# Kernel tuning notes

Hardware: AMD Instinct MI355X
Metric: run time of the kernel (lower is better)

Reference implementation:

```python
import jax, jax.numpy as jnp
import numpy as np

DIM = 1024
HEADS = 16
HEAD_DIM = DIM // HEADS
SCALE = HEAD_DIM ** -0.5


def setup_inputs() -> dict:
    key = jax.random.key(0)
    ks = jax.random.split(key, 6)
    B, N, C = 2, 2048, DIM
    s = C ** -0.5
    return {
        "x": jax.random.normal(ks[0], (B, N, C), dtype=jnp.float32),
        "Wq": jax.random.normal(ks[1], (C, C), dtype=jnp.float32) * s,
        "Wk": jax.random.normal(ks[2], (C, C), dtype=jnp.float32) * s,
        "Wv": jax.random.normal(ks[3], (C, C), dtype=jnp.float32) * s,
        "Wo": jax.random.normal(ks[4], (C, C), dtype=jnp.float32) * s,
        "bo": jax.random.normal(ks[5], (C,), dtype=jnp.float32) * 0.02,
    }


def reference(x, Wq, Wk, Wv, Wo, bo):
    B, N, C = x.shape
    H, D = HEADS, HEAD_DIM
    # q/k/v linears (no bias), reshape to [B, H, N, D]
    q = (x @ Wq.T).reshape(B, N, H, D).transpose(0, 2, 1, 3)
    k = (x @ Wk.T).reshape(B, N, H, D).transpose(0, 2, 1, 3)
    v = (x @ Wv.T).reshape(B, N, H, D).transpose(0, 2, 1, 3)
    attn = jnp.einsum("bhnd,bhmd->bhnm", q, k) * SCALE  # [B,H,N,N]
    attn = jax.nn.softmax(attn, axis=-1)
    out = jnp.einsum("bhnm,bhmd->bhnd", attn, v)  # [B,H,N,D]
    out = out.transpose(0, 2, 1, 3).reshape(B, N, C)
    out = out @ Wo.T + bo  # proj (dropout p=0 in eval -> identity)
    return out
```

## Files before the change

### kernel.cpp

```cpp
#include <hip/hip_runtime.h>
#include <stdint.h>

typedef __attribute__((ext_vector_type(8))) _Float16 half8;
typedef __attribute__((ext_vector_type(8))) unsigned short ushort8;
typedef __attribute__((ext_vector_type(4))) float f32x4;
typedef unsigned short u16;

#define AS1C(p) ((const __attribute__((address_space(1))) void*)(p))
#define AS3(p)  ((__attribute__((address_space(3))) void*)(p))

#define PIPE_WAIT(n) do { asm volatile("s_waitcnt vmcnt(" #n ")" ::: "memory"); \
  __builtin_amdgcn_s_barrier(); __builtin_amdgcn_sched_barrier(0); } while (0)

__device__ __forceinline__ f32x4 mfma_k32(half8 a, half8 b, f32x4 c) {
  return __builtin_amdgcn_mfma_f32_16x16x32_f16(a, b, c, 0, 0, 0);
}
__device__ __forceinline__ u16 f2h(float f) {
  return __builtin_bit_cast(u16, (_Float16)f);
}
__device__ __forceinline__ float fexp2(float x) {
  return __builtin_amdgcn_exp2f(x);
}
__device__ __forceinline__ unsigned int pk2h(float a, float b) {
  return __builtin_bit_cast(unsigned int, __builtin_amdgcn_cvt_pkrtz(a, b));
}
__device__ __forceinline__ int fsz(int r) {
  return (((r & 3) | (((r >> 3) & 1) << 2)) << 4);
}

__global__ __launch_bounds__(256) void k_convert(
    const float* __restrict__ x, const float* __restrict__ wq,
    const float* __restrict__ wk, const float* __restrict__ wv,
    const float* __restrict__ wo,
    u16* __restrict__ xb, u16* __restrict__ wqkvb, u16* __restrict__ wob) {
  size_t t = (size_t)blockIdx.x * 256 + threadIdx.x;
  size_t e = t * 8;
  const float* src;
  u16* dst;
  if (e < 4194304u)      { src = x  + e;            dst = xb    + e; }
  else if (e < 5242880u) { src = wq + (e-4194304u); dst = wqkvb + (e-4194304u); }
  else if (e < 6291456u) { src = wk + (e-5242880u); dst = wqkvb + (e-4194304u); }
  else if (e < 7340032u) { src = wv + (e-6291456u); dst = wqkvb + (e-4194304u); }
  else                   { src = wo + (e-7340032u); dst = wob   + (e-7340032u); }
  float4 a = *(const float4*)src;
  float4 b = *(const float4*)(src + 4);
  ushort8 o;
  o[0]=f2h(a.x); o[1]=f2h(a.y); o[2]=f2h(a.z); o[3]=f2h(a.w);
  o[4]=f2h(b.x); o[5]=f2h(b.y); o[6]=f2h(b.z); o[7]=f2h(b.w);
  *(ushort8*)dst = o;
}

__global__ __launch_bounds__(512) void k_gemm_qkv(
    const u16* __restrict__ xb, const u16* __restrict__ wqkvb,
    u16* __restrict__ qk, u16* __restrict__ vt) {
  __shared__ u16 lA[3 * 4096];
  __shared__ u16 lB[3 * 4096];
  char* lAc = (char*)lA;
  char* lBc = (char*)lB;
  const int lid = blockIdx.x;
  const int xcd = lid & 7, idx = lid >> 3;
  const int pr = idx / 12, pc = idx % 12;
  const int row0 = (((xcd & 3) << 3) + pr) << 7;
  const int col0 = ((xcd >> 2) * 12 + pc) << 7;

  const int tid = threadIdx.x;
  const int w = tid >> 6, lane = tid & 63;
  const int wm = (w & 1) * 64, wn = (w >> 1) * 32;
  const int l15 = lane & 15, l4 = lane >> 4;
  f32x4 acc[4][2];
#pragma unroll
  for (int i = 0; i < 4; ++i)
#pragma unroll
    for (int j = 0; j < 2; ++j) acc[i][j] = (f32x4){0.f, 0.f, 0.f, 0.f};

  const int lrow = lane >> 2;
  const int lcb  = (lane & 3) << 4;
  const char* Abase = (const char*)xb + (size_t)row0 * 2048;
  const char* Bbase = (const char*)wqkvb + (size_t)col0 * 2048;

  auto stage = [&](int buf, int kt) {
    int r = (w << 4) + lrow;
    __builtin_amdgcn_global_load_lds(AS1C(Abase + (size_t)r * 2048 + kt * 64 + lcb),
                                     AS3(lAc + buf * 8192 + w * 1024), 16, 0, 0);
    __builtin_amdgcn_global_load_lds(AS1C(Bbase + (size_t)r * 2048 + kt * 64 + lcb),
                                     AS3(lBc + buf * 8192 + w * 1024), 16, 0, 0);
  };
  auto compute = [&](int buf) {
    const char* A = lAc + buf * 8192;
    const char* B = lBc + buf * 8192;
    half8 af[4], bf[2];
#pragma unroll
    for (int mi = 0; mi < 4; ++mi)
      af[mi] = *(const half8*)(A + (wm + mi * 16 + l15) * 64 + (l4 << 4));
#pragma unroll
    for (int ni = 0; ni < 2; ++ni)
      bf[ni] = *(const half8*)(B + (wn + ni * 16 + l15) * 64 + (l4 << 4));
#pragma unroll
    for (int mi = 0; mi < 4; ++mi)
#pragma unroll
      for (int ni = 0; ni < 2; ++ni)
        acc[mi][ni] = mfma_k32(af[mi], bf[ni], acc[mi][ni]);
  };

  stage(0, 0);
  stage(1, 1);
  for (int k3 = 0; k3 < 30; k3 += 3) {
    PIPE_WAIT(2); stage(2, k3 + 2); compute(0);
    PIPE_WAIT(2); stage(0, k3 + 3); compute(1);
    PIPE_WAIT(2); stage(1, k3 + 4); compute(2);
  }
  PIPE_WAIT(2); compute(0);
  PIPE_WAIT(0); compute(1);

  const int rbase = row0 + wm + (l4 << 2);
  const int cbase = col0 + wn + l15;
  const bool isQ = (col0 < 1024);
  const bool isV = (col0 >= 2048);
#pragma unroll
  for (int mi = 0; mi < 4; ++mi) {
#pragma unroll
    for (int ni = 0; ni < 2; ++ni) {
      const int col = cbase + ni * 16;
      if (!isV) {
#pragma unroll
        for (int r = 0; r < 4; ++r) {
          int row = rbase + mi * 16 + r;
          float v = acc[mi][ni][r];
          if (isQ) v *= 0.18033688f;
          qk[(size_t)row * 2048 + col] = f2h(v);
        }
      } else {
        const int jj = col - 2048;
        const int h = jj >> 6, d = jj & 63;
        const int row = rbase + mi * 16;
        const int b = row >> 11, n = row & 2047;
        u16 pk[4];
#pragma unroll
        for (int r = 0; r < 4; ++r) pk[r] = f2h(acc[mi][ni][r]);
        *(uint2*)&vt[(size_t)(((b << 4) + h) * 64 + d) * 2048 + n] = *(uint2*)pk;
      }
    }
  }
}

__global__ __launch_bounds__(512) void k_attn(
    const u16* __restrict__ qk, const u16* __restrict__ vt, u16* __restrict__ ao) {
  __shared__ u16 KV[6][4096];
  char* L = (char*)&KV[0][0];
  const int lid = blockIdx.x;
  const int xcd = lid & 7, sub = lid >> 3;
  const int bh = (xcd << 2) + (sub >> 4);
  const int qt = sub & 15;
  const int b = bh >> 4, h = bh & 15;
  const int w = threadIdx.x >> 6, lane = threadIdx.x & 63;
  const int l15 = lane & 15, l4 = lane >> 4;

  const int qrow = (b << 11) + (qt << 7) + (w << 4) + l15;
  half8 qf[2];
  qf[0] = *(const half8*)(qk + (size_t)qrow * 2048 + h * 64 + (l4 << 3));
  qf[1] = *(const half8*)(qk + (size_t)qrow * 2048 + h * 64 + 32 + (l4 << 3));

  half8 vones8;
#pragma unroll
  for (int j = 0; j < 8; ++j) vones8[j] = (_Float16)1.0f;

  const int lrow = lane >> 3;
  const int lcb  = (lane & 7) << 4;
  const char* Kbase = (const char*)qk + (size_t)(b << 11) * 4096 + 2048 + h * 128;
  const char* Vbase = (const char*)vt + (size_t)(bh * 64) * 4096;

  const int rr0 = (w << 3) + lrow;
  const int sc0 = lcb ^ fsz(rr0);
  const char* kg0 = Kbase + (size_t)rr0 * 4096 + sc0;
  const char* vg0 = Vbase + (size_t)rr0 * 4096 + sc0;
  const int kd0 = w * 1024;

  const int keybase = ((l15 >> 2) << 3) + (l15 & 3);
  const int kswz = fsz(keybase);
  const int vswz = (((l15 & 3) | (((l15 >> 3) & 1) << 2)) << 4);
  int koff[8], voff[8];
#pragma unroll
  for (int nt = 0; nt < 4; ++nt) {
    const int key = keybase + ((nt & 1) << 2) + ((nt >> 1) << 5);
    koff[2 * nt]     = key * 128 + ((l4 << 4) ^ kswz);
    koff[2 * nt + 1] = key * 128 + (((l4 << 4) + 64) ^ kswz);
  }
#pragma unroll
  for (int dt = 0; dt < 4; ++dt) {
    const int d = dt * 16 + l15;
    voff[2 * dt]     = 24576 + d * 128 + ((l4 << 4) ^ vswz);
    voff[2 * dt + 1] = 24576 + d * 128 + (((l4 << 4) + 64) ^ vswz);
  }

  f32x4 acc_o[4];
  f32x4 acc_l = (f32x4){0.f, 0.f, 0.f, 0.f};
#pragma unroll
  for (int dt = 0; dt < 4; ++dt) acc_o[dt] = (f32x4){0.f, 0.f, 0.f, 0.f};

  auto stage = [&](int buf) {
    __builtin_amdgcn_global_load_lds(AS1C(kg0), AS3(L + buf * 8192 + kd0), 16, 0, 0);
    __builtin_amdgcn_global_load_lds(AS1C(vg0), AS3(L + 24576 + buf * 8192 + kd0), 16, 0, 0);
    kg0 += 262144; vg0 += 128;
  };

  auto compute = [&](int bu) {
    const char* Lb = L + bu * 8192;

    f32x4 s[4];
    __builtin_amdgcn_s_setprio(1);
#pragma unroll
    for (int nt = 0; nt < 4; ++nt) {
      half8 k0 = *(const half8*)(Lb + koff[2 * nt]);
      half8 k1 = *(const half8*)(Lb + koff[2 * nt + 1]);
      f32x4 z = (f32x4){0.f, 0.f, 0.f, 0.f};
      z = mfma_k32(k0, qf[0], z);
      s[nt] = mfma_k32(k1, qf[1], z);
    }
    __builtin_amdgcn_s_setprio(0);

    half8 pb[2];
#pragma unroll
    for (int p = 0; p < 2; ++p) {
      uint4 pk;
      pk.x = pk2h(fexp2(s[2*p][0]),   fexp2(s[2*p][1]));
      pk.y = pk2h(fexp2(s[2*p][2]),   fexp2(s[2*p][3]));
      pk.z = pk2h(fexp2(s[2*p+1][0]), fexp2(s[2*p+1][1]));
      pk.w = pk2h(fexp2(s[2*p+1][2]), fexp2(s[2*p+1][3]));
      pb[p] = __builtin_bit_cast(half8, pk);
    }

    __builtin_amdgcn_s_setprio(1);
#pragma unroll
    for (int dt = 0; dt < 4; ++dt) {
      half8 v0 = *(const half8*)(Lb + voff[2 * dt]);
      half8 v1 = *(const half8*)(Lb + voff[2 * dt + 1]);
      acc_o[dt] = mfma_k32(v0, pb[0], acc_o[dt]);
      acc_o[dt] = mfma_k32(v1, pb[1], acc_o[dt]);
    }
    acc_l = mfma_k32(vones8, pb[0], acc_l);
    acc_l = mfma_k32(vones8, pb[1], acc_l);
    __builtin_amdgcn_s_setprio(0);
  };

  stage(0);
  stage(1);
  for (int k3 = 0; k3 < 30; k3 += 3) {
    PIPE_WAIT(2); stage(2); compute(0);
    PIPE_WAIT(2); stage(0); compute(1);
    PIPE_WAIT(2); stage(1); compute(2);
  }
  PIPE_WAIT(2); compute(0);
  PIPE_WAIT(0); compute(1);

  const float inv = __builtin_amdgcn_rcpf(acc_l[0]);
  const size_t rowbase = ((size_t)(b << 11) + (qt << 7) + (w << 4) + l15) * 1024 + h * 64;
#pragma unroll
  for (int dt = 0; dt < 4; ++dt) {
    uint2 o;
    o.x = pk2h(acc_o[dt][0] * inv, acc_o[dt][1] * inv);
    o.y = pk2h(acc_o[dt][2] * inv, acc_o[dt][3] * inv);
    *(uint2*)&ao[rowbase + dt * 16 + (l4 << 2)] = o;
  }
}

__global__ __launch_bounds__(256) void k_gemm_proj(
    const u16* __restrict__ aob, const u16* __restrict__ wob,
    const float* __restrict__ bo, float* __restrict__ out) {
  __shared__ u16 lA[3 * 4096];
  __shared__ u16 lB[3 * 2048];
  const int lid = blockIdx.x;
  const int xcd = lid & 7, idx = lid >> 3;
  const int row0 = ((xcd << 2) + (idx >> 4)) << 7;
  const int col0 = (idx & 15) << 6;

  const int tid = threadIdx.x;
  const int w = tid >> 6, lane = tid & 63;
  const int wm = (w >> 1) * 64, wn = (w & 1) * 32;
  const int l15 = lane & 15, l4 = lane >> 4;
  f32x4 acc[4][2];
#pragma unroll
  for (int i = 0; i < 4; ++i)
#pragma unroll
    for (int j = 0; j < 2; ++j) acc[i][j] = (f32x4){0.f, 0.f, 0.f, 0.f};

  const int lrow = lane >> 2;
  const int lcb  = (lane & 3) << 4;
  const char* Abase = (const char*)aob + (size_t)row0 * 2048;
  const char* Bbase = (const char*)wob + (size_t)col0 * 2048;
  char* lAc = (char*)lA;
  char* lBc = (char*)lB;

  auto stage = [&](int buf, int kt) {
#pragma unroll
    for (int i = 0; i < 2; ++i) {
      int c = w + 4 * i;
      int r = c * 16 + lrow;
      __builtin_amdgcn_global_load_lds(AS1C(Abase + (size_t)r * 2048 + kt * 64 + lcb),
                                       AS3(lAc + buf * 8192 + c * 1024), 16, 0, 0);
    }
    int rb = w * 16 + lrow;
    __builtin_amdgcn_global_load_lds(AS1C(Bbase + (size_t)rb * 2048 + kt * 64 + lcb),
                                     AS3(lBc + buf * 4096 + w * 1024), 16, 0, 0);
  };
  auto compute = [&](int buf) {
    const char* A = lAc + buf * 8192;
    const char* B = lBc + buf * 4096;
    half8 af[4], bf[2];
#pragma unroll
    for (int mi = 0; mi < 4; ++mi)
      af[mi] = *(const half8*)(A + (wm + mi * 16 + l15) * 64 + (l4 << 4));
#pragma unroll
    for (int ni = 0; ni < 2; ++ni)
      bf[ni] = *(const half8*)(B + (wn + ni * 16 + l15) * 64 + (l4 << 4));
#pragma unroll
    for (int mi = 0; mi < 4; ++mi)
#pragma unroll
      for (int ni = 0; ni < 2; ++ni)
        acc[mi][ni] = mfma_k32(af[mi], bf[ni], acc[mi][ni]);
  };

  stage(0, 0);
  stage(1, 1);
  for (int k3 = 0; k3 < 30; k3 += 3) {
    PIPE_WAIT(3); stage(2, k3 + 2); compute(0);
    PIPE_WAIT(3); stage(0, k3 + 3); compute(1);
    PIPE_WAIT(3); stage(1, k3 + 4); compute(2);
  }
  PIPE_WAIT(3); compute(0);
  PIPE_WAIT(0); compute(1);

  const int rbase = row0 + wm + (l4 << 2);
  const int cbase = col0 + wn + l15;
#pragma unroll
  for (int mi = 0; mi < 4; ++mi) {
#pragma unroll
    for (int ni = 0; ni < 2; ++ni) {
      const int col = cbase + ni * 16;
      const float bb = bo[col];
#pragma unroll
      for (int r = 0; r < 4; ++r) {
        const int row = rbase + mi * 16 + r;
        out[(size_t)row * 1024 + col] = acc[mi][ni][r] + bb;
      }
    }
  }
}

extern "C" void kernel_launch(void* const* d_in, const int* in_sizes, int n_in,
                              void* d_out, int out_size, void* d_ws, size_t ws_size,
                              hipStream_t stream) {
  const float* x  = (const float*)d_in[0];
  const float* wq = (const float*)d_in[1];
  const float* wk = (const float*)d_in[2];
  const float* wv = (const float*)d_in[3];
  const float* wo = (const float*)d_in[4];
  const float* bo = (const float*)d_in[5];
  float* out = (float*)d_out;

  char* ws = (char*)d_ws;
  u16* xb    = (u16*)(ws);
  u16* wqkvb = (u16*)(ws + 8388608);
  u16* wob   = (u16*)(ws + 14680064);
  u16* qkb   = (u16*)(ws + 16777216);
  u16* vtb   = (u16*)(ws + 33554432);
  u16* aob   = (u16*)(ws + 41943040);

  k_convert<<<dim3(4096), dim3(256), 0, stream>>>(x, wq, wk, wv, wo, xb, wqkvb, wob);
  k_gemm_qkv<<<dim3(768), dim3(512), 0, stream>>>(xb, wqkvb, qkb, vtb);
  k_attn<<<dim3(512), dim3(512), 0, stream>>>(qkb, vtb, aob);
  k_gemm_proj<<<dim3(512), dim3(256), 0, stream>>>(aob, wob, bo, out);
}
```

Measured before the change: 108.5 us.

## Process two query subtiles per wave in attention to reuse K/V fragments

The attention kernel now runs 4 waves per block instead of 8, with each wave handling 32 query rows as two 16-row subtiles. K and V fragments are read from LDS once per stage and reused for both subtiles, which halves LDS read traffic per unit of MFMA work. Each thread issues twice as many global-to-LDS loads, so the wait count changes. The cost is higher register pressure (two sets of accumulators and score tiles) and fewer waves per block to hide latency.

```diff
diff --git a/kernel.cpp b/kernel.cpp
--- a/kernel.cpp
+++ b/kernel.cpp
@@ -143,7 +143,7 @@
   }
 }
 
-__global__ __launch_bounds__(512) void k_attn(
+__global__ __launch_bounds__(256) void k_attn(
     const u16* __restrict__ qk, const u16* __restrict__ vt, u16* __restrict__ ao) {
   __shared__ u16 KV[6][4096];
   char* L = (char*)&KV[0][0];
@@ -155,10 +155,13 @@
   const int w = threadIdx.x >> 6, lane = threadIdx.x & 63;
   const int l15 = lane & 15, l4 = lane >> 4;
 
-  const int qrow = (b << 11) + (qt << 7) + (w << 4) + l15;
-  half8 qf[2];
-  qf[0] = *(const half8*)(qk + (size_t)qrow * 2048 + h * 64 + (l4 << 3));
-  qf[1] = *(const half8*)(qk + (size_t)qrow * 2048 + h * 64 + 32 + (l4 << 3));
+  half8 qf[2][2];
+#pragma unroll
+  for (int si = 0; si < 2; ++si) {
+    const int qrow = (b << 11) + (qt << 7) + (w << 5) + (si << 4) + l15;
+    qf[si][0] = *(const half8*)(qk + (size_t)qrow * 2048 + h * 64 + (l4 << 3));
+    qf[si][1] = *(const half8*)(qk + (size_t)qrow * 2048 + h * 64 + 32 + (l4 << 3));
+  }
 
   half8 vones8;
 #pragma unroll
@@ -172,8 +175,10 @@
   const int rr0 = (w << 3) + lrow;
   const int sc0 = lcb ^ fsz(rr0);
   const char* kg0 = Kbase + (size_t)rr0 * 4096 + sc0;
+  const char* kg1 = kg0 + 131072;
   const char* vg0 = Vbase + (size_t)rr0 * 4096 + sc0;
-  const int kd0 = w * 1024;
+  const char* vg1 = vg0 + 131072;
+  const int kd0 = w * 1024, kd1 = (w + 4) * 1024;
 
   const int keybase = ((l15 >> 2) << 3) + (l15 & 3);
   const int kswz = fsz(keybase);
@@ -192,74 +197,93 @@
     voff[2 * dt + 1] = 24576 + d * 128 + (((l4 << 4) + 64) ^ vswz);
   }
 
-  f32x4 acc_o[4];
-  f32x4 acc_l = (f32x4){0.f, 0.f, 0.f, 0.f};
-#pragma unroll
-  for (int dt = 0; dt < 4; ++dt) acc_o[dt] = (f32x4){0.f, 0.f, 0.f, 0.f};
+  f32x4 acc_o[2][4];
+  f32x4 acc_l[2];
+  acc_l[0] = (f32x4){0.f, 0.f, 0.f, 0.f};
+  acc_l[1] = (f32x4){0.f, 0.f, 0.f, 0.f};
+#pragma unroll
+  for (int si = 0; si < 2; ++si)
+#pragma unroll
+    for (int dt = 0; dt < 4; ++dt) acc_o[si][dt] = (f32x4){0.f, 0.f, 0.f, 0.f};
 
   auto stage = [&](int buf) {
     __builtin_amdgcn_global_load_lds(AS1C(kg0), AS3(L + buf * 8192 + kd0), 16, 0, 0);
+    __builtin_amdgcn_global_load_lds(AS1C(kg1), AS3(L + buf * 8192 + kd1), 16, 0, 0);
     __builtin_amdgcn_global_load_lds(AS1C(vg0), AS3(L + 24576 + buf * 8192 + kd0), 16, 0, 0);
-    kg0 += 262144; vg0 += 128;
+    __builtin_amdgcn_global_load_lds(AS1C(vg1), AS3(L + 24576 + buf * 8192 + kd1), 16, 0, 0);
+    kg0 += 262144; kg1 += 262144; vg0 += 128; vg1 += 128;
   };
 
   auto compute = [&](int bu) {
     const char* Lb = L + bu * 8192;
 
-    f32x4 s[4];
+    half8 kf[8];
+#pragma unroll
+    for (int i = 0; i < 8; ++i) kf[i] = *(const half8*)(Lb + koff[i]);
+
+    f32x4 s[2][4];
     __builtin_amdgcn_s_setprio(1);
 #pragma unroll
-    for (int nt = 0; nt < 4; ++nt) {
-      half8 k0 = *(const half8*)(Lb + koff[2 * nt]);
-      half8 k1 = *(const half8*)(Lb + koff[2 * nt + 1]);
-      f32x4 z = (f32x4){0.f, 0.f, 0.f, 0.f};
-      z = mfma_k32(k0, qf[0], z);
-      s[nt] = mfma_k32(k1, qf[1], z);
-    }
+    for (int si = 0; si < 2; ++si)
+#pragma unroll
+      for (int nt = 0; nt < 4; ++nt) {
+        f32x4 z = (f32x4){0.f, 0.f, 0.f, 0.f};
+        z = mfma_k32(kf[2 * nt], qf[si][0], z);
+        s[si][nt] = mfma_k32(kf[2 * nt + 1], qf[si][1], z);
+      }
     __builtin_amdgcn_s_setprio(0);
 
-    half8 pb[2];
-#pragma unroll
-    for (int p = 0; p < 2; ++p) {
-      uint4 pk;
-      pk.x = pk2h(fexp2(s[2*p][0]),   fexp2(s[2*p][1]));
-      pk.y = pk2h(fexp2(s[2*p][2]),   fexp2(s[2*p][3]));
-      pk.z = pk2h(fexp2(s[2*p+1][0]), fexp2(s[2*p+1][1]));
-      pk.w = pk2h(fexp2(s[2*p+1][2]), fexp2(s[2*p+1][3]));
-      pb[p] = __builtin_bit_cast(half8, pk);
-    }
-
-    __builtin_amdgcn_s_setprio(1);
-#pragma unroll
-    for (int dt = 0; dt < 4; ++dt) {
-      half8 v0 = *(const half8*)(Lb + voff[2 * dt]);
-      half8 v1 = *(const half8*)(Lb + voff[2 * dt + 1]);
-      acc_o[dt] = mfma_k32(v0, pb[0], acc_o[dt]);
-      acc_o[dt] = mfma_k32(v1, pb[1], acc_o[dt]);
-    }
-    acc_l = mfma_k32(vones8, pb[0], acc_l);
-    acc_l = mfma_k32(vones8, pb[1], acc_l);
-    __builtin_amdgcn_s_setprio(0);
+    half8 vf[8];
+#pragma unroll
+    for (int i = 0; i < 8; ++i) vf[i] = *(const half8*)(Lb + voff[i]);
+
+#pragma unroll
+    for (int si = 0; si < 2; ++si) {
+      half8 pb[2];
+#pragma unroll
+      for (int p = 0; p < 2; ++p) {
+        uint4 pk;
+        pk.x = pk2h(fexp2(s[si][2*p][0]),   fexp2(s[si][2*p][1]));
+        pk.y = pk2h(fexp2(s[si][2*p][2]),   fexp2(s[si][2*p][3]));
+        pk.z = pk2h(fexp2(s[si][2*p+1][0]), fexp2(s[si][2*p+1][1]));
+        pk.w = pk2h(fexp2(s[si][2*p+1][2]), fexp2(s[si][2*p+1][3]));
+        pb[p] = __builtin_bit_cast(half8, pk);
+      }
+
+      __builtin_amdgcn_s_setprio(1);
+#pragma unroll
+      for (int dt = 0; dt < 4; ++dt) {
+        acc_o[si][dt] = mfma_k32(vf[2 * dt], pb[0], acc_o[si][dt]);
+        acc_o[si][dt] = mfma_k32(vf[2 * dt + 1], pb[1], acc_o[si][dt]);
+      }
+      acc_l[si] = mfma_k32(vones8, pb[0], acc_l[si]);
+      acc_l[si] = mfma_k32(vones8, pb[1], acc_l[si]);
+      __builtin_amdgcn_s_setprio(0);
+    }
   };
 
   stage(0);
   stage(1);
   for (int k3 = 0; k3 < 30; k3 += 3) {
-    PIPE_WAIT(2); stage(2); compute(0);
-    PIPE_WAIT(2); stage(0); compute(1);
-    PIPE_WAIT(2); stage(1); compute(2);
-  }
-  PIPE_WAIT(2); compute(0);
+    PIPE_WAIT(4); stage(2); compute(0);
+    PIPE_WAIT(4); stage(0); compute(1);
+    PIPE_WAIT(4); stage(1); compute(2);
+  }
+  PIPE_WAIT(4); compute(0);
   PIPE_WAIT(0); compute(1);
 
-  const float inv = __builtin_amdgcn_rcpf(acc_l[0]);
-  const size_t rowbase = ((size_t)(b << 11) + (qt << 7) + (w << 4) + l15) * 1024 + h * 64;
-#pragma unroll
-  for (int dt = 0; dt < 4; ++dt) {
-    uint2 o;
-    o.x = pk2h(acc_o[dt][0] * inv, acc_o[dt][1] * inv);
-    o.y = pk2h(acc_o[dt][2] * inv, acc_o[dt][3] * inv);
-    *(uint2*)&ao[rowbase + dt * 16 + (l4 << 2)] = o;
+#pragma unroll
+  for (int si = 0; si < 2; ++si) {
+    const float inv = __builtin_amdgcn_rcpf(acc_l[si][0]);
+    const size_t rowbase =
+        ((size_t)(b << 11) + (qt << 7) + (w << 5) + (si << 4) + l15) * 1024 + h * 64;
+#pragma unroll
+    for (int dt = 0; dt < 4; ++dt) {
+      uint2 o;
+      o.x = pk2h(acc_o[si][dt][0] * inv, acc_o[si][dt][1] * inv);
+      o.y = pk2h(acc_o[si][dt][2] * inv, acc_o[si][dt][3] * inv);
+      *(uint2*)&ao[rowbase + dt * 16 + (l4 << 2)] = o;
+    }
   }
 }
 
@@ -367,6 +391,6 @@
 
   k_convert<<<dim3(4096), dim3(256), 0, stream>>>(x, wq, wk, wv, wo, xb, wqkvb, wob);
   k_gemm_qkv<<<dim3(768), dim3(512), 0, stream>>>(xb, wqkvb, qkb, vtb);
-  k_attn<<<dim3(512), dim3(512), 0, stream>>>(qkb, vtb, aob);
+  k_attn<<<dim3(512), dim3(256), 0, stream>>>(qkb, vtb, aob);
   k_gemm_proj<<<dim3(512), dim3(256), 0, stream>>>(aob, wob, bo, out);
 }
```

Result: no change. 108.7 us (+0.2%).
